# Performance work log

Hardware: AMD Instinct MI355X
Metric: run time of the kernel (lower is better)

## Reference

```python
import jax, jax.numpy as jnp
import numpy as np

B, T, E, V, L = 8, 128, 256, 8192, 5  # batch, block_size, embedding_size (== num heads, head_size=1), vocab, num blocks


def setup_inputs() -> dict:
    key = jax.random.key(0)
    ks = jax.random.split(key, 12)
    s = 0.02
    return {
        "idxs": jax.random.randint(ks[0], (B, T), 0, V),
        "targets": jax.random.randint(ks[1], (B, T), 0, V),
        "emb": jax.random.normal(ks[2], (V, E)) * s,
        "pos_emb": jax.random.normal(ks[3], (T, E)) * s,
        "Wq": jax.random.normal(ks[4], (L, E, E)) * s,  # per-layer: E heads, each Linear(E,1); columns are heads
        "Wk": jax.random.normal(ks[5], (L, E, E)) * s,
        "Wv": jax.random.normal(ks[6], (L, E, E)) * s,
        "Wfc": jax.random.normal(ks[7], (L, E, E)) * s,
        "bfc": jnp.zeros((L, E)),
        "Wlm": jax.random.normal(ks[8], (E, V)) * s,
        "blm": jnp.zeros((V,)),
    }


def _block(x, Wq, Wk, Wv, Wfc, bfc):
    # E heads of head_size=1: projecting with [E,E] gives [B,T,H] with H==E,
    # column h being head h's scalar q/k/v. Faithful to per-head Linear(E,1).
    q = x @ Wq
    k = x @ Wk
    v = x @ Wv
    scores = jnp.einsum('bih,bjh->bhij', q, k)  # no 1/sqrt(d) scaling (faithful)
    i = jnp.arange(x.shape[1])
    causal = i[:, None] >= i[None, :]  # masked_fill where tril==0, i.e. j>i -> -inf
    scores = jnp.where(causal[None, None], scores, -jnp.inf)
    attn = jax.nn.softmax(scores, axis=-2)  # NOTE: source softmaxes over dim=-2 (query axis) -- faithful quirk
    out = jnp.einsum('bhij,bjh->bih', attn, v)  # concat of heads == H axis order
    x = x + out
    return x + jax.nn.relu(x @ Wfc + bfc)


def reference(idxs, targets, emb, pos_emb, Wq, Wk, Wv, Wfc, bfc, Wlm, blm):
    x = emb[idxs] + pos_emb[: idxs.shape[1]]  # [B,T,E]
    for l in range(L):
        x = _block(x, Wq[l], Wk[l], Wv[l], Wfc[l], bfc[l])
    logits = (x @ Wlm + blm).reshape(-1, V)  # [B*T, V], as source views before CE
    logp = jax.nn.log_softmax(logits, axis=-1)
    loss = -jnp.take_along_axis(logp, targets.reshape(-1, 1), axis=-1).mean()
    return logits, loss
```

## Files before the change

kernel.cpp:

```cpp
#include <hip/hip_runtime.h>

#define BB 8
#define TT 128
#define EE 256
#define VV 8192
#define LL 5
#define NROWS (BB*TT)

typedef __attribute__((ext_vector_type(8))) short bf16x8;
typedef __attribute__((ext_vector_type(4))) float f32x4;

__device__ inline ushort f2bf(float f) {
    union { float f; unsigned u; } c; c.f = f;
    unsigned u = c.u;
    return (ushort)((u + 0x7FFF + ((u >> 16) & 1)) >> 16);
}

__global__ __launch_bounds__(256) void prep_kernel(
        const int* __restrict__ idxs, const float* __restrict__ emb, const float* __restrict__ pos,
        const float* __restrict__ Wq, const float* __restrict__ Wk,
        const float* __restrict__ Wv, const float* __restrict__ Wfc,
        const float* __restrict__ Wlm,
        float* __restrict__ x0, ushort* __restrict__ WTs, ushort* __restrict__ WlmT,
        float* __restrict__ loss_cell) {
    int id = blockIdx.x;
    if (id == 0) {
        if (threadIdx.x == 0) *loss_cell = 0.f;
        return;
    }
    if (id < 513) {
        __shared__ ushort ts[64][72];
        int idw = id - 1;
        int v0 = (idw & 127) * 64, k0 = (idw >> 7) * 64;
        int lane = threadIdx.x & 63, w = threadIdx.x >> 6;
        for (int kk = w; kk < 64; kk += 4)
            ts[lane][kk] = f2bf(Wlm[(size_t)(k0 + kk)*VV + v0 + lane]);
        __syncthreads();
        for (int vv = w; vv < 64; vv += 4)
            WlmT[(size_t)(v0 + vv)*EE + k0 + lane] = ts[vv][lane];
        return;
    }
    if (id < 833) {
        __shared__ ushort ts[64][72];
        int idm = id - 513;
        int mat = idm >> 4, tile = idm & 15;
        int l = mat >> 2, type = mat & 3;
        const float* src = (type == 0 ? Wq : type == 1 ? Wk : type == 2 ? Wv : Wfc) + l*EE*EE;
        ushort* dst = WTs + mat*EE*EE;
        int i0 = (tile >> 2) * 64, o0 = (tile & 3) * 64;
        int lane = threadIdx.x & 63, w = threadIdx.x >> 6;
        for (int ii = w; ii < 64; ii += 4)
            ts[lane][ii] = f2bf(src[(i0 + ii)*EE + o0 + lane]);
        __syncthreads();
        for (int oo = w; oo < 64; oo += 4)
            dst[(o0 + oo)*EE + i0 + lane] = ts[oo][lane];
        return;
    }
    int h = threadIdx.x;
    int row0 = (id - 833) * 4;
    for (int r = 0; r < 4; ++r) {
        int row = row0 + r;
        x0[row*EE + h] = emb[(size_t)idxs[row]*EE + h] + pos[(row & (TT-1))*EE + h];
    }
}

__global__ __launch_bounds__(512) void qkv_attn_kernel(
        float* __restrict__ x, const ushort* __restrict__ WTl) {
    __shared__ __align__(16) ushort Xs[128*256];
    __shared__ __align__(16) ushort Bs[32*256];
    __shared__ float QS[8*132], KS[8*132], VS[8*132], MS[8*132], RV[8*132];
    int tid = threadIdx.x, lane = tid & 63, w = tid >> 6;
    int b  = blockIdx.x >> 5;
    int h0 = (blockIdx.x & 31) * 8;

    for (int rr = w; rr < 128; rr += 8) {
        float4 v = *(const float4*)&x[(size_t)(b*TT + rr)*EE + lane*4];
        ushort4 hh; hh.x = f2bf(v.x); hh.y = f2bf(v.y); hh.z = f2bf(v.z); hh.w = f2bf(v.w);
        *(ushort4*)&Xs[rr*256 + ((lane*4) ^ ((rr & 7) << 3))] = hh;
    }
    {
        int c = tid >> 4;
        int kb = (tid & 15) * 16;
        uint4 v0 = make_uint4(0,0,0,0), v1 = v0;
        if (c < 24) {
            int mat = c >> 3;
            int col = h0 + (c & 7);
            const ushort* src = WTl + (size_t)mat*EE*EE + (size_t)col*EE + kb;
            v0 = *(const uint4*)&src[0];
            v1 = *(const uint4*)&src[8];
        }
        *(uint4*)&Bs[c*256 + (kb ^ ((c & 7) << 3))] = v0;
        *(uint4*)&Bs[c*256 + ((kb + 8) ^ ((c & 7) << 3))] = v1;
    }
    __syncthreads();

    {
        f32x4 acc[2] = {};
        int rband = w*16 + (lane & 15);
        int kq = (lane >> 4) * 8;
        for (int ks = 0; ks < 8; ++ks) {
            int kk = ks*32 + kq;
            bf16x8 a = *(const bf16x8*)&Xs[rband*256 + (kk ^ ((rband & 7) << 3))];
            #pragma unroll
            for (int ct = 0; ct < 2; ++ct) {
                int c = ct*16 + (lane & 15);
                bf16x8 bb = *(const bf16x8*)&Bs[c*256 + (kk ^ ((c & 7) << 3))];
                acc[ct] = __builtin_amdgcn_mfma_f32_16x16x32_bf16(a, bb, acc[ct], 0, 0, 0);
            }
        }
        int r_ = w*16 + ((lane >> 4) << 2);
        #pragma unroll
        for (int ct = 0; ct < 2; ++ct) {
            int col24 = ct*16 + (lane & 15);
            #pragma unroll
            for (int j = 0; j < 4; ++j) {
                float val = acc[ct][j];
                int row = r_ + j;
                if (col24 < 8)       QS[col24*132 + row] = val;
                else if (col24 < 16) KS[(col24-8)*132 + row] = val;
                else if (col24 < 24) VS[(col24-16)*132 + row] = val;
            }
        }
    }
    __syncthreads();

    int g = w, lg = lane;
    {
        int j0 = lg*2;
        float k0 = KS[g*132 + j0], k1 = KS[g*132 + j0 + 1];
        float m0 = -INFINITY, m1 = -INFINITY;
        for (int i = j0; i < TT; ++i) {
            float qi = QS[g*132 + i];
            m0 = fmaxf(m0, qi*k0);
            m1 = (i >= j0+1) ? fmaxf(m1, qi*k1) : m1;
        }
        float z0 = 0.f, z1 = 0.f;
        for (int i = j0; i < TT; ++i) {
            float qi = QS[g*132 + i];
            z0 += __expf(qi*k0 - m0);
            z1 += (i >= j0+1) ? __expf(qi*k1 - m1) : 0.f;
        }
        MS[g*132 + j0]     = m0;
        MS[g*132 + j0 + 1] = m1;
        RV[g*132 + j0]     = VS[g*132 + j0] / z0;
        RV[g*132 + j0 + 1] = VS[g*132 + j0 + 1] / z1;
    }
    __syncthreads();
    float a0 = 0.f, a1 = 0.f;
    {
        int i0 = lg*2;
        float q0 = QS[g*132 + i0], q1 = QS[g*132 + i0 + 1];
        for (int j = 0; j <= i0 + 1; ++j) {
            float kj = KS[g*132 + j], mj = MS[g*132 + j], rj = RV[g*132 + j];
            float e0 = __expf(q0*kj - mj) * rj;
            float e1 = __expf(q1*kj - mj) * rj;
            a0 += (j <= i0) ? e0 : 0.f;
            a1 += e1;
        }
    }
    __syncthreads();
    VS[g*132 + lg*2]     = a0;
    VS[g*132 + lg*2 + 1] = a1;
    __syncthreads();

    {
        int row = tid >> 2, cp = (tid & 3) * 2;
        size_t gx = (size_t)(b*TT + row)*EE + h0 + cp;
        float2 xv = *(float2*)&x[gx];
        xv.x += VS[cp*132 + row];
        xv.y += VS[(cp+1)*132 + row];
        *(float2*)&x[gx] = xv;
    }
}

__global__ __launch_bounds__(256) void fc_mfma(
        const float* __restrict__ xin, const ushort* __restrict__ WT,
        const float* __restrict__ bfc, float* __restrict__ xout) {
    __shared__ __align__(16) ushort As[64*256];
    __shared__ __align__(16) ushort Bs[64*256];
    int tid = threadIdx.x, lane = tid & 63, w = tid >> 6;
    int c0 = blockIdx.x * 64;
    int r0 = blockIdx.y * 64;

    for (int rr = w; rr < 64; rr += 4) {
        float4 v = *(const float4*)&xin[(size_t)(r0 + rr)*EE + lane*4];
        ushort4 hh; hh.x = f2bf(v.x); hh.y = f2bf(v.y); hh.z = f2bf(v.z); hh.w = f2bf(v.w);
        *(ushort4*)&As[rr*256 + ((lane*4) ^ ((rr & 7) << 3))] = hh;
    }
    for (int it = 0; it < 8; ++it) {
        int c = w*16 + (lane >> 5) + 2*it;
        int k0i = (lane & 31) * 8;
        uint4 v = *(const uint4*)&WT[(size_t)(c0 + c)*EE + k0i];
        *(uint4*)&Bs[c*256 + (k0i ^ ((c & 7) << 3))] = v;
    }
    __syncthreads();
    f32x4 acc[4] = {};
    int rband = w*16 + (lane & 15);
    int kq = (lane >> 4) * 8;
    for (int ks = 0; ks < 8; ++ks) {
        int kk = ks*32 + kq;
        bf16x8 a = *(const bf16x8*)&As[rband*256 + (kk ^ ((rband & 7) << 3))];
        #pragma unroll
        for (int n = 0; n < 4; ++n) {
            int c = n*16 + (lane & 15);
            bf16x8 b = *(const bf16x8*)&Bs[c*256 + (kk ^ ((c & 7) << 3))];
            acc[n] = __builtin_amdgcn_mfma_f32_16x16x32_bf16(a, b, acc[n], 0, 0, 0);
        }
    }
    int grow0 = r0 + w*16 + ((lane >> 4) << 2);
    #pragma unroll
    for (int n = 0; n < 4; ++n) {
        int col = c0 + n*16 + (lane & 15);
        float bias = bfc[col];
        #pragma unroll
        for (int j = 0; j < 4; ++j) {
            size_t idx = (size_t)(grow0 + j)*EE + col;
            xout[idx] = xin[idx] + fmaxf(acc[n][j] + bias, 0.f);
        }
    }
}

__global__ __launch_bounds__(256) void lm_mfma_kernel(
        const float* __restrict__ x, const ushort* __restrict__ WlmT,
        const float* __restrict__ blm, float* __restrict__ out,
        float* __restrict__ pm, float* __restrict__ pz) {
    __shared__ __align__(16) ushort As[64*256];
    __shared__ __align__(16) ushort Bs[64*256];
    int tid = threadIdx.x;
    int lane = tid & 63, w = tid >> 6;
    int c0 = blockIdx.x * 64;
    int r0 = blockIdx.y * 64;

    for (int rr = w; rr < 64; rr += 4) {
        float4 v = *(const float4*)&x[(size_t)(r0 + rr)*EE + lane*4];
        ushort4 hh; hh.x = f2bf(v.x); hh.y = f2bf(v.y); hh.z = f2bf(v.z); hh.w = f2bf(v.w);
        *(ushort4*)&As[rr*256 + ((lane*4) ^ ((rr & 7) << 3))] = hh;
    }
    for (int it = 0; it < 8; ++it) {
        int c = w*16 + (lane >> 5) + 2*it;
        int k0i = (lane & 31) * 8;
        uint4 v = *(const uint4*)&WlmT[(size_t)(c0 + c)*EE + k0i];
        *(uint4*)&Bs[c*256 + (k0i ^ ((c & 7) << 3))] = v;
    }
    __syncthreads();

    f32x4 acc[4] = {};
    int rband = w*16 + (lane & 15);
    int kq = (lane >> 4) * 8;
    for (int ks = 0; ks < 8; ++ks) {
        int kk = ks*32 + kq;
        bf16x8 a = *(const bf16x8*)&As[rband*256 + (kk ^ ((rband & 7) << 3))];
        #pragma unroll
        for (int n = 0; n < 4; ++n) {
            int c = n*16 + (lane & 15);
            bf16x8 b = *(const bf16x8*)&Bs[c*256 + (kk ^ ((c & 7) << 3))];
            acc[n] = __builtin_amdgcn_mfma_f32_16x16x32_bf16(a, b, acc[n], 0, 0, 0);
        }
    }
    __syncthreads();

    float* fst = (float*)As;
    float bias[4];
    #pragma unroll
    for (int n = 0; n < 4; ++n) bias[n] = blm[c0 + n*16 + (lane & 15)];
    int rw = w*16 + (lane >> 4)*4;
    int rowg = r0 + rw;
    #pragma unroll
    for (int j = 0; j < 4; ++j) {
        float vals[4];
        float vmax = -INFINITY;
        #pragma unroll
        for (int n = 0; n < 4; ++n) {
            vals[n] = acc[n][j] + bias[n];
            fst[(rw + j)*68 + n*16 + (lane & 15)] = vals[n];
            vmax = fmaxf(vmax, vals[n]);
        }
        #pragma unroll
        for (int m = 1; m <= 8; m <<= 1) vmax = fmaxf(vmax, __shfl_xor(vmax, m));
        float z = 0.f;
        #pragma unroll
        for (int n = 0; n < 4; ++n) z += __expf(vals[n] - vmax);
        #pragma unroll
        for (int m = 1; m <= 8; m <<= 1) z += __shfl_xor(z, m);
        if ((lane & 15) == 0) {
            pm[(size_t)(rowg + j)*128 + blockIdx.x] = vmax;
            pz[(size_t)(rowg + j)*128 + blockIdx.x] = z;
        }
    }
    __syncthreads();
    #pragma unroll
    for (int it = 0; it < 4; ++it) {
        int k = tid + it*256;
        int row = k >> 4, c4 = (k & 15)*4;
        float4 v = *(float4*)&fst[row*68 + c4];
        *(float4*)&out[(size_t)(r0 + row)*VV + c0 + c4] = v;
    }
}

__global__ void loss_kernel(const float* __restrict__ pm, const float* __restrict__ pz,
                            const float* __restrict__ logits, const int* __restrict__ targets,
                            float* __restrict__ out_last) {
    int r = blockIdx.x;
    int t = threadIdx.x;
    __shared__ float sm[128], sz[128];
    float m = pm[(size_t)r*128 + t];
    float z = pz[(size_t)r*128 + t];
    sm[t] = m; __syncthreads();
    for (int s = 64; s > 0; s >>= 1) {
        if (t < s) sm[t] = fmaxf(sm[t], sm[t + s]);
        __syncthreads();
    }
    float M = sm[0];
    sz[t] = z * __expf(m - M); __syncthreads();
    for (int s = 64; s > 0; s >>= 1) {
        if (t < s) sz[t] += sz[t + s];
        __syncthreads();
    }
    if (t == 0) {
        float lse = M + logf(sz[0]);
        atomicAdd(out_last, (lse - logits[(size_t)r*VV + targets[r]]) * (1.0f / NROWS));
    }
}

extern "C" void kernel_launch(void* const* d_in, const int* in_sizes, int n_in,
                              void* d_out, int out_size, void* d_ws, size_t ws_size,
                              hipStream_t stream) {
    const int*   idxs    = (const int*)d_in[0];
    const int*   targets = (const int*)d_in[1];
    const float* emb     = (const float*)d_in[2];
    const float* pos     = (const float*)d_in[3];
    const float* Wq      = (const float*)d_in[4];
    const float* Wk      = (const float*)d_in[5];
    const float* Wv      = (const float*)d_in[6];
    const float* Wfc     = (const float*)d_in[7];
    const float* bfc     = (const float*)d_in[8];
    const float* Wlm     = (const float*)d_in[9];
    const float* blm     = (const float*)d_in[10];
    float* out = (float*)d_out;
    float* loss_cell = out + (size_t)NROWS * VV;

    float* ws = (float*)d_ws;
    float*  xa   = ws;
    float*  xb   = xa + NROWS*EE;
    float*  pm   = xb + NROWS*EE;
    float*  pz   = pm + NROWS*128;
    ushort* WTs  = (ushort*)(pz + NROWS*128);
    ushort* WlmT = WTs + 20*EE*EE;

    prep_kernel<<<1089, 256, 0, stream>>>(idxs, emb, pos, Wq, Wk, Wv, Wfc, Wlm,
                                          xa, WTs, WlmT, loss_cell);

    for (int l = 0; l < LL; ++l) {
        float* xi = (l & 1) ? xb : xa;
        float* xo = (l & 1) ? xa : xb;
        qkv_attn_kernel<<<256, 512, 0, stream>>>(xi, WTs + (size_t)l*4*EE*EE);
        fc_mfma<<<dim3(4, 16), 256, 0, stream>>>(xi, WTs + (size_t)(l*4 + 3)*EE*EE,
                                                 bfc + l*EE, xo);
    }

    lm_mfma_kernel<<<dim3(VV/64, NROWS/64), 256, 0, stream>>>(xb, WlmT, blm, out, pm, pz);
    loss_kernel<<<NROWS, 128, 0, stream>>>(pm, pz, out, targets, loss_cell);
}
```

Baseline: 241.8 us.

## Enlarge LM-head tiles to 128x128 and compute causal max via suffix min/max

The LM-head GEMM moves from 64x64 tiles with 256 threads to 128x128 tiles with 512 threads. Each wave now computes a 64x32 sub-tile, so its A and B fragments are reused across more MFMAs. The partial max/sum buffers double to 256 per row, and the loss kernel is widened to match. Separately, the per-key softmax max in attention no longer loops over all queries: it uses a wave-level suffix max/min of q, exploiting max(q*k) = k*max(q) or k*min(q) depending on the sign of k. The trade-off is fewer, larger blocks using much more LDS, which lowers occupancy and leaves fewer blocks to spread over the CUs.

```diff
diff --git a/kernel.cpp b/kernel.cpp
--- a/kernel.cpp
+++ b/kernel.cpp
@@ -128,12 +128,19 @@
     {
         int j0 = lg*2;
         float k0 = KS[g*132 + j0], k1 = KS[g*132 + j0 + 1];
-        float m0 = -INFINITY, m1 = -INFINITY;
-        for (int i = j0; i < TT; ++i) {
-            float qi = QS[g*132 + i];
-            m0 = fmaxf(m0, qi*k0);
-            m1 = (i >= j0+1) ? fmaxf(m1, qi*k1) : m1;
-        }
+        float q0j = QS[g*132 + j0], q1j = QS[g*132 + j0 + 1];
+        float pmax = fmaxf(q0j, q1j), pmin = fminf(q0j, q1j);
+        #pragma unroll
+        for (int d = 1; d < 64; d <<= 1) {
+            float om = __shfl_down(pmax, d);
+            float on = __shfl_down(pmin, d);
+            if (lg + d < 64) { pmax = fmaxf(pmax, om); pmin = fminf(pmin, on); }
+        }
+        float nx = __shfl_down(pmax, 1), nn = __shfl_down(pmin, 1);
+        float sp1 = (lg == 63) ? q1j : fmaxf(q1j, nx);
+        float sn1 = (lg == 63) ? q1j : fminf(q1j, nn);
+        float m0 = (k0 >= 0.f) ? k0*pmax : k0*pmin;
+        float m1 = (k1 >= 0.f) ? k1*sp1  : k1*sn1;
         float z0 = 0.f, z1 = 0.f;
         for (int i = j0; i < TT; ++i) {
             float qi = QS[g*132 + i];
@@ -220,18 +227,19 @@
     }
 }
 
-__global__ __launch_bounds__(256) void lm_mfma_kernel(
+__global__ __launch_bounds__(512) void lm_mfma_kernel(
         const float* __restrict__ x, const ushort* __restrict__ WlmT,
         const float* __restrict__ blm, float* __restrict__ out,
         float* __restrict__ pm, float* __restrict__ pz) {
-    __shared__ __align__(16) ushort As[64*256];
-    __shared__ __align__(16) ushort Bs[64*256];
+    __shared__ __align__(16) ushort LDSb[2*128*256];
+    ushort* As = LDSb;
+    ushort* Bs = LDSb + 128*256;
     int tid = threadIdx.x;
     int lane = tid & 63, w = tid >> 6;
-    int c0 = blockIdx.x * 64;
-    int r0 = blockIdx.y * 64;
-
-    for (int rr = w; rr < 64; rr += 4) {
+    int c0 = blockIdx.x * 128;
+    int r0 = blockIdx.y * 128;
+
+    for (int rr = w; rr < 128; rr += 8) {
         float4 v = *(const float4*)&x[(size_t)(r0 + rr)*EE + lane*4];
         ushort4 hh; hh.x = f2bf(v.x); hh.y = f2bf(v.y); hh.z = f2bf(v.z); hh.w = f2bf(v.w);
         *(ushort4*)&As[rr*256 + ((lane*4) ^ ((rr & 7) << 3))] = hh;
@@ -244,55 +252,67 @@
     }
     __syncthreads();
 
-    f32x4 acc[4] = {};
-    int rband = w*16 + (lane & 15);
+    int wr = (w >> 2) * 64, wc = (w & 3) * 32;
+    f32x4 acc[4][2] = {};
     int kq = (lane >> 4) * 8;
     for (int ks = 0; ks < 8; ++ks) {
         int kk = ks*32 + kq;
-        bf16x8 a = *(const bf16x8*)&As[rband*256 + (kk ^ ((rband & 7) << 3))];
-        #pragma unroll
-        for (int n = 0; n < 4; ++n) {
-            int c = n*16 + (lane & 15);
-            bf16x8 b = *(const bf16x8*)&Bs[c*256 + (kk ^ ((c & 7) << 3))];
-            acc[n] = __builtin_amdgcn_mfma_f32_16x16x32_bf16(a, b, acc[n], 0, 0, 0);
-        }
-    }
-    __syncthreads();
-
-    float* fst = (float*)As;
-    float bias[4];
+        bf16x8 a[4], bfr[2];
+        #pragma unroll
+        for (int m = 0; m < 4; ++m) {
+            int rband = wr + m*16 + (lane & 15);
+            a[m] = *(const bf16x8*)&As[rband*256 + (kk ^ ((rband & 7) << 3))];
+        }
+        #pragma unroll
+        for (int n = 0; n < 2; ++n) {
+            int c = wc + n*16 + (lane & 15);
+            bfr[n] = *(const bf16x8*)&Bs[c*256 + (kk ^ ((c & 7) << 3))];
+        }
+        #pragma unroll
+        for (int m = 0; m < 4; ++m)
+            #pragma unroll
+            for (int n = 0; n < 2; ++n)
+                acc[m][n] = __builtin_amdgcn_mfma_f32_16x16x32_bf16(a[m], bfr[n], acc[m][n], 0, 0, 0);
+    }
+    __syncthreads();
+
+    float* fst = (float*)LDSb;
+    float bias[2];
     #pragma unroll
-    for (int n = 0; n < 4; ++n) bias[n] = blm[c0 + n*16 + (lane & 15)];
-    int rw = w*16 + (lane >> 4)*4;
-    int rowg = r0 + rw;
+    for (int n = 0; n < 2; ++n) bias[n] = blm[c0 + wc + n*16 + (lane & 15)];
     #pragma unroll
-    for (int j = 0; j < 4; ++j) {
-        float vals[4];
-        float vmax = -INFINITY;
-        #pragma unroll
-        for (int n = 0; n < 4; ++n) {
-            vals[n] = acc[n][j] + bias[n];
-            fst[(rw + j)*68 + n*16 + (lane & 15)] = vals[n];
-            vmax = fmaxf(vmax, vals[n]);
-        }
-        #pragma unroll
-        for (int m = 1; m <= 8; m <<= 1) vmax = fmaxf(vmax, __shfl_xor(vmax, m));
-        float z = 0.f;
-        #pragma unroll
-        for (int n = 0; n < 4; ++n) z += __expf(vals[n] - vmax);
-        #pragma unroll
-        for (int m = 1; m <= 8; m <<= 1) z += __shfl_xor(z, m);
-        if ((lane & 15) == 0) {
-            pm[(size_t)(rowg + j)*128 + blockIdx.x] = vmax;
-            pz[(size_t)(rowg + j)*128 + blockIdx.x] = z;
+    for (int m = 0; m < 4; ++m) {
+        int rw = wr + m*16 + (lane >> 4)*4;
+        #pragma unroll
+        for (int j = 0; j < 4; ++j) {
+            int row = rw + j;
+            float vals[2];
+            float vmax = -INFINITY;
+            #pragma unroll
+            for (int n = 0; n < 2; ++n) {
+                vals[n] = acc[m][n][j] + bias[n];
+                fst[row*132 + wc + n*16 + (lane & 15)] = vals[n];
+                vmax = fmaxf(vmax, vals[n]);
+            }
+            #pragma unroll
+            for (int msk = 1; msk <= 8; msk <<= 1) vmax = fmaxf(vmax, __shfl_xor(vmax, msk));
+            float z = 0.f;
+            #pragma unroll
+            for (int n = 0; n < 2; ++n) z += __expf(vals[n] - vmax);
+            #pragma unroll
+            for (int msk = 1; msk <= 8; msk <<= 1) z += __shfl_xor(z, msk);
+            if ((lane & 15) == 0) {
+                pm[(size_t)(r0 + row)*256 + blockIdx.x*4 + (w & 3)] = vmax;
+                pz[(size_t)(r0 + row)*256 + blockIdx.x*4 + (w & 3)] = z;
+            }
         }
     }
     __syncthreads();
     #pragma unroll
-    for (int it = 0; it < 4; ++it) {
-        int k = tid + it*256;
-        int row = k >> 4, c4 = (k & 15)*4;
-        float4 v = *(float4*)&fst[row*68 + c4];
+    for (int it = 0; it < 8; ++it) {
+        int k = tid + it*512;
+        int row = k >> 5, c4 = (k & 31)*4;
+        float4 v = *(float4*)&fst[row*132 + c4];
         *(float4*)&out[(size_t)(r0 + row)*VV + c0 + c4] = v;
     }
 }
@@ -302,17 +322,17 @@
                             float* __restrict__ out_last) {
     int r = blockIdx.x;
     int t = threadIdx.x;
-    __shared__ float sm[128], sz[128];
-    float m = pm[(size_t)r*128 + t];
-    float z = pz[(size_t)r*128 + t];
+    __shared__ float sm[256], sz[256];
+    float m = pm[(size_t)r*256 + t];
+    float z = pz[(size_t)r*256 + t];
     sm[t] = m; __syncthreads();
-    for (int s = 64; s > 0; s >>= 1) {
+    for (int s = 128; s > 0; s >>= 1) {
         if (t < s) sm[t] = fmaxf(sm[t], sm[t + s]);
         __syncthreads();
     }
     float M = sm[0];
     sz[t] = z * __expf(m - M); __syncthreads();
-    for (int s = 64; s > 0; s >>= 1) {
+    for (int s = 128; s > 0; s >>= 1) {
         if (t < s) sz[t] += sz[t + s];
         __syncthreads();
     }
@@ -343,8 +363,8 @@
     float*  xa   = ws;
     float*  xb   = xa + NROWS*EE;
     float*  pm   = xb + NROWS*EE;
-    float*  pz   = pm + NROWS*128;
-    ushort* WTs  = (ushort*)(pz + NROWS*128);
+    float*  pz   = pm + NROWS*256;
+    ushort* WTs  = (ushort*)(pz + NROWS*256);
     ushort* WlmT = WTs + 20*EE*EE;
 
     prep_kernel<<<1089, 256, 0, stream>>>(idxs, emb, pos, Wq, Wk, Wv, Wfc, Wlm,
@@ -358,6 +378,6 @@
                                                  bfc + l*EE, xo);
     }
 
-    lm_mfma_kernel<<<dim3(VV/64, NROWS/64), 256, 0, stream>>>(xb, WlmT, blm, out, pm, pz);
-    loss_kernel<<<NROWS, 128, 0, stream>>>(pm, pz, out, targets, loss_cell);
-}
+    lm_mfma_kernel<<<dim3(VV/128, NROWS/128), 512, 0, stream>>>(xb, WlmT, blm, out, pm, pz);
+    loss_kernel<<<NROWS, 256, 0, stream>>>(pm, pz, out, targets, loss_cell);
+}
```

Measured after the change: 208.1 us. -13.9%, faster.
